# Kernel optimization log

Hardware: AMD Instinct MI355X
Metric: run time of the kernel (lower is better)

Reference implementation:

```python
import jax, jax.numpy as jnp
import numpy as np
from jax import lax

DIM = 256
HEADS = 8
SR = 2
LN_EPS = 1e-6


def setup_inputs() -> dict:
    key = jax.random.key(0)
    ks = jax.random.split(key, 6)
    B, N, C = 4, 4096, DIM
    x = jax.random.normal(ks[0], (B, N, C), dtype=jnp.float32)
    Wq = jax.random.normal(ks[1], (C, DIM), dtype=jnp.float32) * (C ** -0.5)
    bq = jnp.zeros((DIM,), dtype=jnp.float32)
    Wconv = jax.random.normal(ks[2], (SR, SR, C, DIM), dtype=jnp.float32) * ((SR * SR * C) ** -0.5)
    bconv = jnp.zeros((DIM,), dtype=jnp.float32)
    ln_scale = jnp.ones((DIM,), dtype=jnp.float32)
    ln_bias = jnp.zeros((DIM,), dtype=jnp.float32)
    Wkv = jax.random.normal(ks[3], (DIM, 2 * DIM), dtype=jnp.float32) * (DIM ** -0.5)
    bkv = jnp.zeros((2 * DIM,), dtype=jnp.float32)
    Wproj = jax.random.normal(ks[4], (DIM, DIM), dtype=jnp.float32) * (DIM ** -0.5)
    bproj = jnp.zeros((DIM,), dtype=jnp.float32)
    return {"x": x, "Wq": Wq, "bq": bq, "Wconv": Wconv, "bconv": bconv,
            "ln_scale": ln_scale, "ln_bias": ln_bias, "Wkv": Wkv, "bkv": bkv,
            "Wproj": Wproj, "bproj": bproj}


def reference(x, Wq, bq, Wconv, bconv, ln_scale, ln_bias, Wkv, bkv, Wproj, bproj):
    B, N, C = x.shape
    H = W = int(N ** 0.5)
    head_dim = C // HEADS
    scale = head_dim ** -0.5

    # Q projection: [B, HEADS, N, head_dim]
    q = (x @ Wq + bq).reshape(B, N, HEADS, head_dim).transpose(0, 2, 1, 3)

    # Spatial reduction for K/V (faithful to source: transpose to (B,C,N) then reshape to NHWC)
    xi = jnp.transpose(x, (0, 2, 1)).reshape(B, H, W, C)
    # kernel==stride and H % SR == 0 -> flax SAME padding adds zero padding, same as VALID
    conv = lax.conv_general_dilated(xi, Wconv, window_strides=(SR, SR), padding='VALID',
                                    dimension_numbers=('NHWC', 'HWIO', 'NHWC')) + bconv
    conv = conv.reshape(B, -1, C)  # [B, N/SR^2, C]

    # LayerNorm (flax default eps=1e-6)
    mu = jnp.mean(conv, axis=-1, keepdims=True)
    var = jnp.mean(jnp.square(conv - mu), axis=-1, keepdims=True)
    norm = (conv - mu) * lax.rsqrt(var + LN_EPS) * ln_scale + ln_bias

    # KV projection: kv -> [2, B, HEADS, N_kv, head_dim]
    kv = (norm @ Wkv + bkv).reshape(B, -1, 2, HEADS, head_dim).transpose(2, 0, 3, 1, 4)
    k, v = kv[0], kv[1]

    # Attention (scale applied after q@k^T, as in source)
    att = jnp.einsum('bhqd,bhkd->bhqk', q, k) * scale
    att = jax.nn.softmax(att, axis=-1)
    out = jnp.einsum('bhqk,bhkd->bhqd', att, v)
    out = out.transpose(0, 2, 1, 3).reshape(B, N, C)
    return out @ Wproj + bproj
```

## Files before the change

### kernel.cpp

```cpp
#include <hip/hip_runtime.h>
#include <hip/hip_bf16.h>
#include <stdint.h>


typedef __attribute__((ext_vector_type(8))) short short8;
typedef __attribute__((ext_vector_type(4))) short short4v;
typedef __attribute__((ext_vector_type(2))) float f32x2;
typedef __attribute__((ext_vector_type(2))) unsigned int u32x2;
typedef __attribute__((ext_vector_type(4))) float f32x4;
typedef __attribute__((ext_vector_type(16))) float f32x16;

#define AS1 __attribute__((address_space(1)))
#define AS3 __attribute__((address_space(3)))

static __device__ __forceinline__ unsigned short f2bfu(float f) {
  __hip_bfloat16 h = __float2bfloat16(f);
  unsigned short u; __builtin_memcpy(&u, &h, 2); return u;
}

static __device__ __forceinline__ float fast_exp2(float x) {
#if __has_builtin(__builtin_amdgcn_exp2f)
  return __builtin_amdgcn_exp2f(x);
#else
  return __expf(x * 0.6931471805599453f);
#endif
}

static __device__ __forceinline__ unsigned int pkbf(float lo, float hi) {
  unsigned int ulo = __builtin_bit_cast(unsigned int, lo) + 0x8000u;
  unsigned int uhi = __builtin_bit_cast(unsigned int, hi) + 0x8000u;
  return __builtin_amdgcn_perm(uhi, ulo, 0x07060302u);
}
static __device__ __forceinline__ unsigned int pkbf_t(float lo, float hi) {
  return __builtin_amdgcn_perm(__builtin_bit_cast(unsigned int, hi),
                               __builtin_bit_cast(unsigned int, lo), 0x07060302u);
}

__global__ __launch_bounds__(256) void k_prep(const float* __restrict__ x,
                                              unsigned short* __restrict__ xbf,
                                              unsigned short* __restrict__ A,
                                              const float* __restrict__ Wq, const float* __restrict__ Wconv,
                                              const float* __restrict__ Wkv, const float* __restrict__ Wproj,
                                              unsigned short* __restrict__ WqT, unsigned short* __restrict__ WconvT,
                                              unsigned short* __restrict__ WkvT, unsigned short* __restrict__ WprojT) {
  __shared__ unsigned short tile[64][258];
  int blk = blockIdx.x;
  int t = threadIdx.x;
  if (blk >= 256) {
    int i = (blk - 256) * 256 + t;
    const float* src; unsigned short* dst; int K, N, j;
    if (i < 65536)       { src = Wq;    dst = WqT;    K = 256;  N = 256; j = i; }
    else if (i < 327680) { src = Wconv; dst = WconvT; K = 1024; N = 256; j = i - 65536; }
    else if (i < 458752) { src = Wkv;   dst = WkvT;   K = 256;  N = 512; j = i - 327680; }
    else                 { src = Wproj; dst = WprojT; K = 256;  N = 256; j = i - 458752; }
    int n = j / K, k = j % K;
    dst[j] = f2bfu(src[(size_t)k * N + n]);
    return;
  }
  int b    = blk >> 6;
  int wlow = (blk >> 2) & 15;
  int cib  = blk & 3;
  int ci0  = cib << 6;
  {
    int i = t >> 2, c0 = (t & 3) << 6;
    size_t row = (size_t)(b * 4096 + wlow * 256 + ci0 + i);
    const float* xr = x + row * 256 + c0;
    unsigned short* xw = xbf + row * 256 + c0;
#pragma unroll
    for (int j = 0; j < 16; ++j) {
      f32x4 v = *(const f32x4*)(xr + j * 4);
      short4v ov;
      ov[0] = (short)f2bfu(v[0]); ov[1] = (short)f2bfu(v[1]);
      ov[2] = (short)f2bfu(v[2]); ov[3] = (short)f2bfu(v[3]);
      tile[i][c0 + j*4 + 0] = (unsigned short)ov[0];
      tile[i][c0 + j*4 + 1] = (unsigned short)ov[1];
      tile[i][c0 + j*4 + 2] = (unsigned short)ov[2];
      tile[i][c0 + j*4 + 3] = (unsigned short)ov[3];
      *(short4v*)(xw + j * 4) = ov;
    }
  }
  __syncthreads();
  int wv = t >> 6, lane = t & 63;
#pragma unroll 4
  for (int rep = 0; rep < 64; ++rep) {
    int c = rep * 4 + wv;
    int h = c >> 2;
    int w = ((c & 3) << 4) + wlow;
    int row = b * 1024 + (h >> 1) * 32 + (w >> 1);
    int col = ((h & 1) << 9) + ((w & 1) << 8) + ci0 + lane;
    A[(size_t)row * 1024 + col] = tile[lane][c];
  }
}

__global__ __launch_bounds__(256) void k_gemmqc(const unsigned short* __restrict__ xbf,
                                                const unsigned short* __restrict__ WqT,
                                                const float* __restrict__ bq,
                                                unsigned short* __restrict__ qbf,
                                                const unsigned short* __restrict__ Ac,
                                                const unsigned short* __restrict__ WcT,
                                                const float* __restrict__ bc,
                                                float* __restrict__ convf,
                                                float c1) {
  __shared__ __attribute__((aligned(16))) unsigned short As[64 * 32];
  __shared__ __attribute__((aligned(16))) unsigned short Bs[128 * 32];
  int bid = blockIdx.x, t = threadIdx.x;
  int wave = t >> 6, lane = t & 63;
  const unsigned short *A, *Bt; const float* bias;
  int K, m0, n0, kbeg, z; bool isQ;
  if (bid < 512) {
    isQ = true; z = 0;
    A = xbf; Bt = WqT; bias = bq; K = 256;
    m0 = (bid >> 1) << 6; n0 = (bid & 1) << 7; kbeg = 0;
  } else {
    isQ = false;
    int j = bid - 512; z = j >> 7; int r = j & 127;
    A = Ac; Bt = WcT; bias = bc; K = 1024;
    m0 = (r >> 1) << 6; n0 = (r & 1) << 7; kbeg = z << 8;
  }
  int kend = kbeg + 256;
  int lr = lane & 15, lk = (lane >> 4) << 3;
  f32x4 acc[4][2] = {};
  for (int k0 = kbeg; k0 < kend; k0 += 32) {
    __syncthreads();
    {
      int row = t >> 2, kc = (t & 3) << 3;
      __builtin_amdgcn_global_load_lds((const AS1 unsigned int*)(A + (size_t)(m0 + row) * K + k0 + kc),
                                       (AS3 unsigned int*)(As + t * 8), 16, 0, 0);
    }
#pragma unroll
    for (int it = 0; it < 2; ++it) {
      int c = it * 256 + t;
      int row = c >> 2, kc = (c & 3) << 3;
      __builtin_amdgcn_global_load_lds((const AS1 unsigned int*)(Bt + (size_t)(n0 + row) * K + k0 + kc),
                                       (AS3 unsigned int*)(Bs + c * 8), 16, 0, 0);
    }
    __syncthreads();
    short8 af[4], bfr[2];
#pragma unroll
    for (int mi = 0; mi < 4; ++mi) af[mi]  = *(const short8*)(As + (mi*16 + lr)*32 + lk);
#pragma unroll
    for (int ni = 0; ni < 2; ++ni) bfr[ni] = *(const short8*)(Bs + (wave*32 + ni*16 + lr)*32 + lk);
#pragma unroll
    for (int mi = 0; mi < 4; ++mi)
#pragma unroll
      for (int ni = 0; ni < 2; ++ni)
        acc[mi][ni] = __builtin_amdgcn_mfma_f32_16x16x32_bf16(af[mi], bfr[ni], acc[mi][ni], 0, 0, 0);
  }
  int lrow = (lane >> 4) << 2, lcol = lane & 15;
#pragma unroll
  for (int mi = 0; mi < 4; ++mi) {
#pragma unroll
    for (int ni = 0; ni < 2; ++ni) {
      int gm = m0 + mi*16 + lrow;
      int gn = n0 + wave*32 + ni*16 + lcol;
      float bv = (z == 0) ? bias[gn] : 0.f;
#pragma unroll
      for (int r = 0; r < 4; ++r) {
        float v = acc[mi][ni][r] + bv;
        if (isQ) qbf[(size_t)(gm + r) * 256 + gn] = f2bfu(v * c1);
        else     convf[(size_t)z * 1048576 + (size_t)(gm + r) * 256 + gn] = v;
      }
    }
  }
}

__global__ __launch_bounds__(256) void k_gemm(const unsigned short* __restrict__ A,
                                              const unsigned short* __restrict__ Bt,
                                              const float* __restrict__ bias,
                                              unsigned short* __restrict__ Cb,
                                              float* __restrict__ Cf,
                                              unsigned short* __restrict__ VFout,
                                              int M, int N, int K, int mode, float oscale) {
  __shared__ __attribute__((aligned(16))) unsigned short As[64 * 32];
  __shared__ __attribute__((aligned(16))) unsigned short Bs[128 * 32];
  int t = threadIdx.x;
  int wave = t >> 6, lane = t & 63;
  int m0 = blockIdx.x << 6, n0 = blockIdx.y << 7;
  int lr = lane & 15, lk = (lane >> 4) << 3;
  f32x4 acc[4][2] = {};
  for (int k0 = 0; k0 < K; k0 += 32) {
    __syncthreads();
    {
      int row = t >> 2, kc = (t & 3) << 3;
      __builtin_amdgcn_global_load_lds((const AS1 unsigned int*)(A + (size_t)(m0 + row) * K + k0 + kc),
                                       (AS3 unsigned int*)(As + t * 8), 16, 0, 0);
    }
#pragma unroll
    for (int it = 0; it < 2; ++it) {
      int c = it * 256 + t;
      int row = c >> 2, kc = (c & 3) << 3;
      __builtin_amdgcn_global_load_lds((const AS1 unsigned int*)(Bt + (size_t)(n0 + row) * K + k0 + kc),
                                       (AS3 unsigned int*)(Bs + c * 8), 16, 0, 0);
    }
    __syncthreads();
    short8 af[4], bfr[2];
#pragma unroll
    for (int mi = 0; mi < 4; ++mi) af[mi]  = *(const short8*)(As + (mi*16 + lr)*32 + lk);
#pragma unroll
    for (int ni = 0; ni < 2; ++ni) bfr[ni] = *(const short8*)(Bs + (wave*32 + ni*16 + lr)*32 + lk);
#pragma unroll
    for (int mi = 0; mi < 4; ++mi)
#pragma unroll
      for (int ni = 0; ni < 2; ++ni)
        acc[mi][ni] = __builtin_amdgcn_mfma_f32_16x16x32_bf16(af[mi], bfr[ni], acc[mi][ni], 0, 0, 0);
  }
  int lrow = (lane >> 4) << 2, lcol = lane & 15;
#pragma unroll
  for (int mi = 0; mi < 4; ++mi) {
#pragma unroll
    for (int ni = 0; ni < 2; ++ni) {
      int gm = m0 + mi*16 + lrow;
      int gn = n0 + wave*32 + ni*16 + lcol;
      float bv = bias[gn];
#pragma unroll
      for (int r = 0; r < 4; ++r) {
        float v = acc[mi][ni][r] + bv;
        if (mode == 1) Cf[(size_t)(gm + r) * N + gn] = v;
        else {
          int tok = gm + r;
          int bb = tok >> 10, k10 = tok & 1023;
          int chunk = k10 >> 5, kc2 = k10 & 31;
          if (gn < 256) {
            int hh = gn >> 5, dd = gn & 31;
            int fr = dd >> 4, hi2 = (dd >> 3) & 1, j = dd & 7;
            size_t base = (((size_t)(bb * 8 + hh) * 32 + chunk) * 2 + fr) * 512;
            Cb[base + (hi2 * 32 + kc2) * 8 + j] = f2bfu(v);
          } else {
            int hh = (gn - 256) >> 5, dd = (gn - 256) & 31;
            int pos = (kc2 & 16) | (((kc2 >> 2) & 1) << 3) | (((kc2 >> 3) & 1) << 2) | (kc2 & 3);
            int fr = pos >> 4, hi2 = (pos >> 3) & 1, tt = pos & 7;
            size_t base = (((size_t)(bb * 8 + hh) * 32 + chunk) * 2 + fr) * 512;
            VFout[base + (hi2 * 32 + dd) * 8 + tt] = f2bfu(v);
          }
        }
      }
    }
  }
}

__global__ __launch_bounds__(256) void k_ln(const float* __restrict__ conv,
                                            const float* __restrict__ gamma,
                                            const float* __restrict__ beta,
                                            unsigned short* __restrict__ out) {
  int row = (blockIdx.x << 2) + (threadIdx.x >> 6);
  int lane = threadIdx.x & 63;
  const float* r0 = conv + (size_t)row * 256 + lane * 4;
  f32x4 v = *(const f32x4*)r0;
  v += *(const f32x4*)(r0 + 1048576);
  v += *(const f32x4*)(r0 + 2097152);
  v += *(const f32x4*)(r0 + 3145728);
  float s = v[0] + v[1] + v[2] + v[3];
#pragma unroll
  for (int m = 1; m < 64; m <<= 1) s += __shfl_xor(s, m);
  float mu = s * (1.f / 256.f);
  f32x4 d; float qv = 0.f;
#pragma unroll
  for (int j = 0; j < 4; ++j) { d[j] = v[j] - mu; qv += d[j] * d[j]; }
#pragma unroll
  for (int m = 1; m < 64; m <<= 1) qv += __shfl_xor(qv, m);
  float rstd = rsqrtf(qv * (1.f / 256.f) + 1e-6f);
  f32x4 g  = *(const f32x4*)(gamma + lane * 4);
  f32x4 bb = *(const f32x4*)(beta  + lane * 4);
  short4v ov;
#pragma unroll
  for (int j = 0; j < 4; ++j) ov[j] = (short)f2bfu(d[j] * rstd * g[j] + bb[j]);
  *(short4v*)(out + (size_t)row * 256 + lane * 4) = ov;
}

__global__ __launch_bounds__(256) void k_attn(const unsigned short* __restrict__ qb,
                                              const unsigned short* __restrict__ KF,
                                              const unsigned short* __restrict__ VF,
                                              unsigned short* __restrict__ o) {
  __shared__ float comb[2][64][34];
  int flat = blockIdx.y * 32 + blockIdx.x;
  int bh = (flat & 7) * 4 + (flat >> 8);
  int qg = (flat >> 3) & 31;
  int b = bh >> 3, h = bh & 7;
  int wave = threadIdx.x >> 6, lane = threadIdx.x & 63;
  int qs = wave & 1, kvh = wave >> 1;
  int q0 = (qg * 2 + qs) * 64;
  int lq = lane & 31, hi = lane >> 5;
  const unsigned short* qrA = qb + (size_t)(b * 4096 + q0 + lq) * 256 + h * 32 + hi * 8;
  short8 QA0 = *(const short8*)(qrA);
  short8 QA1 = *(const short8*)(qrA + 16);
  short8 QB0 = *(const short8*)(qrA + 32 * 256);
  short8 QB1 = *(const short8*)(qrA + 32 * 256 + 16);
  const unsigned short* kf = KF + (size_t)bh * 32768 + (size_t)kvh * 16384 + lane * 8;
  const unsigned short* vf = VF + (size_t)bh * 32768 + (size_t)kvh * 16384 + lane * 8;
  const short sone = (short)0x3F80;
  short8 ones = {sone, sone, sone, sone, sone, sone, sone, sone};
  f32x16 accA = {}, accB = {}, alsA = {}, alsB = {};
  short8 Kc0 = *(const short8*)(kf), Kc1 = *(const short8*)(kf + 512);
  short8 Vc0 = *(const short8*)(vf), Vc1 = *(const short8*)(vf + 512);
  for (int c = 0; c < 16; ++c) {
    int no = (c == 15) ? 0 : (c + 1) * 1024;
    short8 Kn0 = *(const short8*)(kf + no), Kn1 = *(const short8*)(kf + no + 512);
    short8 Vn0 = *(const short8*)(vf + no), Vn1 = *(const short8*)(vf + no + 512);
    f32x16 z = {};
    __builtin_amdgcn_s_setprio(1);
    f32x16 sA = __builtin_amdgcn_mfma_f32_32x32x16_bf16(Kc0, QA0, z, 0, 0, 0);
    sA = __builtin_amdgcn_mfma_f32_32x32x16_bf16(Kc1, QA1, sA, 0, 0, 0);
    f32x16 sB = __builtin_amdgcn_mfma_f32_32x32x16_bf16(Kc0, QB0, z, 0, 0, 0);
    sB = __builtin_amdgcn_mfma_f32_32x32x16_bf16(Kc1, QB1, sB, 0, 0, 0);
    __builtin_amdgcn_s_setprio(0);
    union { unsigned int u[4]; short8 s8; } fA0, fA1, fB0, fB1;
#pragma unroll
    for (int w = 0; w < 4; ++w) {
      fA0.u[w] = pkbf_t(fast_exp2(sA[2*w]),     fast_exp2(sA[2*w + 1]));
      fA1.u[w] = pkbf_t(fast_exp2(sA[8 + 2*w]), fast_exp2(sA[9 + 2*w]));
      fB0.u[w] = pkbf_t(fast_exp2(sB[2*w]),     fast_exp2(sB[2*w + 1]));
      fB1.u[w] = pkbf_t(fast_exp2(sB[8 + 2*w]), fast_exp2(sB[9 + 2*w]));
    }
    __builtin_amdgcn_s_setprio(1);
    accA = __builtin_amdgcn_mfma_f32_32x32x16_bf16(Vc0, fA0.s8, accA, 0, 0, 0);
    accA = __builtin_amdgcn_mfma_f32_32x32x16_bf16(Vc1, fA1.s8, accA, 0, 0, 0);
    accB = __builtin_amdgcn_mfma_f32_32x32x16_bf16(Vc0, fB0.s8, accB, 0, 0, 0);
    accB = __builtin_amdgcn_mfma_f32_32x32x16_bf16(Vc1, fB1.s8, accB, 0, 0, 0);
    alsA = __builtin_amdgcn_mfma_f32_32x32x16_bf16(ones, fA0.s8, alsA, 0, 0, 0);
    alsA = __builtin_amdgcn_mfma_f32_32x32x16_bf16(ones, fA1.s8, alsA, 0, 0, 0);
    alsB = __builtin_amdgcn_mfma_f32_32x32x16_bf16(ones, fB0.s8, alsB, 0, 0, 0);
    alsB = __builtin_amdgcn_mfma_f32_32x32x16_bf16(ones, fB1.s8, alsB, 0, 0, 0);
    __builtin_amdgcn_s_setprio(0);
    Kc0 = Kn0; Kc1 = Kn1; Vc0 = Vn0; Vc1 = Vn1;
  }
  float lsA = alsA[0], lsB = alsB[0];
  if (kvh) {
    float* dst = &comb[qs][lane][0];
#pragma unroll
    for (int r = 0; r < 16; r += 2) {
      *(f32x2*)&dst[r]      = (f32x2){accA[r], accA[r+1]};
      *(f32x2*)&dst[16 + r] = (f32x2){accB[r], accB[r+1]};
    }
    *(f32x2*)&dst[32] = (f32x2){lsA, lsB};
  }
  __syncthreads();
  if (!kvh) {
    const float* src = &comb[qs][lane][0];
#pragma unroll
    for (int r = 0; r < 16; ++r) { accA[r] += src[r]; accB[r] += src[16 + r]; }
    lsA += src[32]; lsB += src[33];
    float invA = 1.f / lsA, invB = 1.f / lsB;
    unsigned short* orA = o + (size_t)(b * 4096 + q0 + lq) * 256 + h * 32 + 4 * hi;
    unsigned short* orB = orA + (size_t)32 * 256;
#pragma unroll
    for (int g = 0; g < 4; ++g) {
      u32x2 ovA, ovB;
      ovA[0] = pkbf(accA[4*g+0] * invA, accA[4*g+1] * invA);
      ovA[1] = pkbf(accA[4*g+2] * invA, accA[4*g+3] * invA);
      ovB[0] = pkbf(accB[4*g+0] * invB, accB[4*g+1] * invB);
      ovB[1] = pkbf(accB[4*g+2] * invB, accB[4*g+3] * invB);
      *(u32x2*)(orA + 8 * g) = ovA;
      *(u32x2*)(orB + 8 * g) = ovB;
    }
  }
}

extern "C" void kernel_launch(void* const* d_in, const int* in_sizes, int n_in,
                              void* d_out, int out_size, void* d_ws, size_t ws_size,
                              hipStream_t stream) {
  const float* x     = (const float*)d_in[0];
  const float* Wq    = (const float*)d_in[1];
  const float* bq    = (const float*)d_in[2];
  const float* Wconv = (const float*)d_in[3];
  const float* bconv = (const float*)d_in[4];
  const float* ln_s  = (const float*)d_in[5];
  const float* ln_b  = (const float*)d_in[6];
  const float* Wkv   = (const float*)d_in[7];
  const float* bkv   = (const float*)d_in[8];
  const float* Wproj = (const float*)d_in[9];
  const float* bproj = (const float*)d_in[10];

  char* ws = (char*)d_ws;
  unsigned short* x_bf   = (unsigned short*)(ws);
  unsigned short* VF     = (unsigned short*)(ws);
  unsigned short* q_bf   = (unsigned short*)(ws + (size_t)(8  << 20));
  unsigned short* Aconv  = (unsigned short*)(ws + (size_t)(16 << 20));
  unsigned short* attn_o = Aconv;
  float*          conv_f = (float*)(ws + (size_t)(24 << 20));
  unsigned short* norm_b = (unsigned short*)(ws + (size_t)(40 << 20));
  unsigned short* KF     = (unsigned short*)(ws + (size_t)(42 << 20));
  unsigned short* WqT    = (unsigned short*)(ws + (size_t)(44 << 20));
  unsigned short* WconvT = WqT + 65536;
  unsigned short* WkvT   = WconvT + 262144;
  unsigned short* WprojT = WkvT + 131072;

  const float c1 = (float)(0.17677669529663687 * 1.4426950408889634);

  k_prep<<<2304, 256, 0, stream>>>(x, x_bf, Aconv, Wq, Wconv, Wkv, Wproj,
                                   WqT, WconvT, WkvT, WprojT);
  k_gemmqc<<<1024, 256, 0, stream>>>(x_bf, WqT, bq, q_bf,
                                     Aconv, WconvT, bconv, conv_f, c1);
  k_ln<<<1024, 256, 0, stream>>>(conv_f, ln_s, ln_b, norm_b);
  k_gemm<<<dim3(64, 4), 256, 0, stream>>>(norm_b, WkvT, bkv, KF, nullptr, VF, 4096, 512, 256, 2, 1.f);
  k_attn<<<dim3(32, 32), 256, 0, stream>>>(q_bf, KF, VF, attn_o);
  k_gemm<<<dim3(256, 2), 256, 0, stream>>>(attn_o, WprojT, bproj, nullptr, (float*)d_out, nullptr, 16384, 256, 256, 1, 1.f);
}
```

Before: 86.02 us.

## Tile weight transpose through LDS and software-pipeline QK^T ahead of softmax

Weight conversion in the prep kernel now transposes 64x64 tiles through shared memory, so both global reads and writes are coalesced. This replaces the old one-element-per-thread strided gather and cuts the prep grid from 2304 to 384 blocks. The attention loop is also software-pipelined: the score MFMAs for the next KV chunk are issued before the exp/PV work of the current chunk, with the first chunk peeled off and a drain step at the end. The aim is to overlap MFMA latency with the exp2 VALU work, at the cost of more registers for the extra score accumulators.

```diff
diff --git a/kernel.cpp b/kernel.cpp
--- a/kernel.cpp
+++ b/kernel.cpp
@@ -47,14 +47,35 @@
   int blk = blockIdx.x;
   int t = threadIdx.x;
   if (blk >= 256) {
-    int i = (blk - 256) * 256 + t;
-    const float* src; unsigned short* dst; int K, N, j;
-    if (i < 65536)       { src = Wq;    dst = WqT;    K = 256;  N = 256; j = i; }
-    else if (i < 327680) { src = Wconv; dst = WconvT; K = 1024; N = 256; j = i - 65536; }
-    else if (i < 458752) { src = Wkv;   dst = WkvT;   K = 256;  N = 512; j = i - 327680; }
-    else                 { src = Wproj; dst = WprojT; K = 256;  N = 256; j = i - 458752; }
-    int n = j / K, k = j % K;
-    dst[j] = f2bfu(src[(size_t)k * N + n]);
+    int ti = blk - 256;
+    const float* src; unsigned short* dst; int K, N, tk, tn;
+    if (ti < 16)      { src = Wq;    dst = WqT;    K = 256;  N = 256; tk = ti >> 2;        tn = ti & 3; }
+    else if (ti < 80) { src = Wconv; dst = WconvT; K = 1024; N = 256; int j = ti - 16;  tk = j >> 2; tn = j & 3; }
+    else if (ti <112) { src = Wkv;   dst = WkvT;   K = 256;  N = 512; int j = ti - 80;  tk = j >> 3; tn = j & 7; }
+    else              { src = Wproj; dst = WprojT; K = 256;  N = 256; int j = ti - 112; tk = j >> 2; tn = j & 3; }
+    int k0 = tk << 6, n0 = tn << 6;
+    float* ft = (float*)&tile[0][0];
+    {
+      int row = t >> 2, c4 = (t & 3) << 4;
+      const float* sp = src + (size_t)(k0 + row) * N + n0 + c4;
+#pragma unroll
+      for (int j = 0; j < 4; ++j)
+        *(f32x4*)&ft[row * 65 + c4 + j * 4] = *(const f32x4*)(sp + j * 4);
+    }
+    __syncthreads();
+    {
+      int n = t >> 2, k4 = (t & 3) << 4;
+      unsigned short* dp = dst + (size_t)(n0 + n) * K + k0 + k4;
+#pragma unroll
+      for (int j = 0; j < 16; j += 4) {
+        short4v o;
+        o[0] = (short)f2bfu(ft[(k4 + j + 0) * 65 + n]);
+        o[1] = (short)f2bfu(ft[(k4 + j + 1) * 65 + n]);
+        o[2] = (short)f2bfu(ft[(k4 + j + 2) * 65 + n]);
+        o[3] = (short)f2bfu(ft[(k4 + j + 3) * 65 + n]);
+        *(short4v*)(dp + j) = o;
+      }
+    }
     return;
   }
   int b    = blk >> 6;
@@ -290,19 +311,26 @@
   const short sone = (short)0x3F80;
   short8 ones = {sone, sone, sone, sone, sone, sone, sone, sone};
   f32x16 accA = {}, accB = {}, alsA = {}, alsB = {};
-  short8 Kc0 = *(const short8*)(kf), Kc1 = *(const short8*)(kf + 512);
-  short8 Vc0 = *(const short8*)(vf), Vc1 = *(const short8*)(vf + 512);
-  for (int c = 0; c < 16; ++c) {
-    int no = (c == 15) ? 0 : (c + 1) * 1024;
-    short8 Kn0 = *(const short8*)(kf + no), Kn1 = *(const short8*)(kf + no + 512);
-    short8 Vn0 = *(const short8*)(vf + no), Vn1 = *(const short8*)(vf + no + 512);
-    f32x16 z = {};
+  f32x16 z = {};
+  short8 Ka0 = *(const short8*)(kf), Ka1 = *(const short8*)(kf + 512);
+  f32x16 sA = __builtin_amdgcn_mfma_f32_32x32x16_bf16(Ka0, QA0, z, 0, 0, 0);
+  sA = __builtin_amdgcn_mfma_f32_32x32x16_bf16(Ka1, QA1, sA, 0, 0, 0);
+  f32x16 sB = __builtin_amdgcn_mfma_f32_32x32x16_bf16(Ka0, QB0, z, 0, 0, 0);
+  sB = __builtin_amdgcn_mfma_f32_32x32x16_bf16(Ka1, QB1, sB, 0, 0, 0);
+  short8 Kc0 = *(const short8*)(kf + 1024), Kc1 = *(const short8*)(kf + 1536);
+  short8 Vc0 = *(const short8*)(vf),        Vc1 = *(const short8*)(vf + 512);
+  for (int c = 0; c < 15; ++c) {
+    int kno = (c == 14) ? 0 : (c + 2) * 1024;
+    int vno = (c + 1) * 1024;
+    short8 Kn0 = *(const short8*)(kf + kno), Kn1 = *(const short8*)(kf + kno + 512);
+    short8 Vn0 = *(const short8*)(vf + vno), Vn1 = *(const short8*)(vf + vno + 512);
     __builtin_amdgcn_s_setprio(1);
-    f32x16 sA = __builtin_amdgcn_mfma_f32_32x32x16_bf16(Kc0, QA0, z, 0, 0, 0);
-    sA = __builtin_amdgcn_mfma_f32_32x32x16_bf16(Kc1, QA1, sA, 0, 0, 0);
-    f32x16 sB = __builtin_amdgcn_mfma_f32_32x32x16_bf16(Kc0, QB0, z, 0, 0, 0);
-    sB = __builtin_amdgcn_mfma_f32_32x32x16_bf16(Kc1, QB1, sB, 0, 0, 0);
+    f32x16 sAn = __builtin_amdgcn_mfma_f32_32x32x16_bf16(Kc0, QA0, z, 0, 0, 0);
+    sAn = __builtin_amdgcn_mfma_f32_32x32x16_bf16(Kc1, QA1, sAn, 0, 0, 0);
+    f32x16 sBn = __builtin_amdgcn_mfma_f32_32x32x16_bf16(Kc0, QB0, z, 0, 0, 0);
+    sBn = __builtin_amdgcn_mfma_f32_32x32x16_bf16(Kc1, QB1, sBn, 0, 0, 0);
     __builtin_amdgcn_s_setprio(0);
+    __builtin_amdgcn_sched_barrier(0);
     union { unsigned int u[4]; short8 s8; } fA0, fA1, fB0, fB1;
 #pragma unroll
     for (int w = 0; w < 4; ++w) {
@@ -321,7 +349,26 @@
     alsB = __builtin_amdgcn_mfma_f32_32x32x16_bf16(ones, fB0.s8, alsB, 0, 0, 0);
     alsB = __builtin_amdgcn_mfma_f32_32x32x16_bf16(ones, fB1.s8, alsB, 0, 0, 0);
     __builtin_amdgcn_s_setprio(0);
+    sA = sAn; sB = sBn;
     Kc0 = Kn0; Kc1 = Kn1; Vc0 = Vn0; Vc1 = Vn1;
+  }
+  {
+    union { unsigned int u[4]; short8 s8; } fA0, fA1, fB0, fB1;
+#pragma unroll
+    for (int w = 0; w < 4; ++w) {
+      fA0.u[w] = pkbf_t(fast_exp2(sA[2*w]),     fast_exp2(sA[2*w + 1]));
+      fA1.u[w] = pkbf_t(fast_exp2(sA[8 + 2*w]), fast_exp2(sA[9 + 2*w]));
+      fB0.u[w] = pkbf_t(fast_exp2(sB[2*w]),     fast_exp2(sB[2*w + 1]));
+      fB1.u[w] = pkbf_t(fast_exp2(sB[8 + 2*w]), fast_exp2(sB[9 + 2*w]));
+    }
+    accA = __builtin_amdgcn_mfma_f32_32x32x16_bf16(Vc0, fA0.s8, accA, 0, 0, 0);
+    accA = __builtin_amdgcn_mfma_f32_32x32x16_bf16(Vc1, fA1.s8, accA, 0, 0, 0);
+    accB = __builtin_amdgcn_mfma_f32_32x32x16_bf16(Vc0, fB0.s8, accB, 0, 0, 0);
+    accB = __builtin_amdgcn_mfma_f32_32x32x16_bf16(Vc1, fB1.s8, accB, 0, 0, 0);
+    alsA = __builtin_amdgcn_mfma_f32_32x32x16_bf16(ones, fA0.s8, alsA, 0, 0, 0);
+    alsA = __builtin_amdgcn_mfma_f32_32x32x16_bf16(ones, fA1.s8, alsA, 0, 0, 0);
+    alsB = __builtin_amdgcn_mfma_f32_32x32x16_bf16(ones, fB0.s8, alsB, 0, 0, 0);
+    alsB = __builtin_amdgcn_mfma_f32_32x32x16_bf16(ones, fB1.s8, alsB, 0, 0, 0);
   }
   float lsA = alsA[0], lsB = alsB[0];
   if (kvh) {
@@ -386,8 +433,8 @@
 
   const float c1 = (float)(0.17677669529663687 * 1.4426950408889634);
 
-  k_prep<<<2304, 256, 0, stream>>>(x, x_bf, Aconv, Wq, Wconv, Wkv, Wproj,
-                                   WqT, WconvT, WkvT, WprojT);
+  k_prep<<<384, 256, 0, stream>>>(x, x_bf, Aconv, Wq, Wconv, Wkv, Wproj,
+                                  WqT, WconvT, WkvT, WprojT);
   k_gemmqc<<<1024, 256, 0, stream>>>(x_bf, WqT, bq, q_bf,
                                      Aconv, WconvT, bconv, conv_f, c1);
   k_ln<<<1024, 256, 0, stream>>>(conv_f, ln_s, ln_b, norm_b);
```

New measurement: 81.94 us (median of 2 runs). -4.7%, faster.
